# Kernel tuning notes

Hardware: AMD Instinct MI355X
Metric: run time of the kernel (lower is better)

Reference implementation:

```python
import jax, jax.numpy as jnp
import numpy as np

K = 2  # max_diffusion_step
UNITS = 128
NUM_NODES = 1024


def _diffusion_conv(x, support, W, b):
    # x: (B, N, D) ; Chebyshev diffusion over scaled Laplacian support (N, N)
    x0 = x
    x1 = jnp.einsum('nm,bmd->bnd', support, x0)
    xs = [x0, x1]
    for _ in range(K - 1):
        xs.append(2.0 * jnp.einsum('nm,bmd->bnd', support, xs[-1]) - xs[-2])
    feats = jnp.concatenate(xs, axis=-1)  # (B, N, D*(K+1))
    return feats @ W + b


def _gclstm_cell(x, h, c, support, W, b):
    gates = _diffusion_conv(jnp.concatenate([x, h], axis=-1), support, W, b)
    i, f, o, g = jnp.split(gates, 4, axis=-1)
    c_new = jax.nn.sigmoid(f) * c + jax.nn.sigmoid(i) * jnp.tanh(g)
    h_new = jax.nn.sigmoid(o) * jnp.tanh(c_new)
    return h_new, c_new


def setup_inputs() -> dict:
    key = jax.random.key(0)
    ks = jax.random.split(key, 8)
    B, S, N, H = 64, 12, NUM_NODES, UNITS

    # build scaled-Laplacian support from a sparse random symmetric adjacency
    rng = np.random.default_rng(0)
    A = (rng.random((N, N)) < 0.01).astype(np.float32)
    A = np.maximum(A, A.T)
    np.fill_diagonal(A, 0.0)
    d = A.sum(axis=1)
    d_is = 1.0 / np.sqrt(np.maximum(d, 1.0))
    L = np.eye(N, dtype=np.float32) - (d_is[:, None] * A * d_is[None, :])
    support = (L - np.eye(N, dtype=np.float32)).astype(np.float32)  # lambda_max ~ 2

    def lin(k, shape, fan_in):
        return jax.random.normal(k, shape, jnp.float32) / np.sqrt(fan_in)

    return {
        'inputs': jax.random.normal(ks[0], (B, N, 1), jnp.float32),
        'encoder_outputs': jax.random.normal(ks[1], (S, B, N, H), jnp.float32),
        'hidden_state': jax.random.normal(ks[2], (2, B, N, H), jnp.float32),
        'cell_state': jax.random.normal(ks[3], (2, B, N, H), jnp.float32),
        'supports': jnp.asarray(support),
        'w0': lin(ks[4], ((1 + H) * (K + 1), 4 * H), (1 + H) * (K + 1)),
        'b0': jnp.zeros((4 * H,), jnp.float32),
        'w1': lin(ks[5], ((H + H) * (K + 1), 4 * H), 2 * H * (K + 1)),
        'b1': jnp.zeros((4 * H,), jnp.float32),
        'attn_w': lin(ks[6], (H, H), H),
        'attn_b': jnp.zeros((H,), jnp.float32),
        'proj_w': lin(ks[7], (2 * H, 1), 2 * H),
        'proj_b': jnp.zeros((1,), jnp.float32),
    }


def reference(inputs, encoder_outputs, hidden_state, cell_state, supports,
              w0, b0, w1, b1, attn_w, attn_b, proj_w, proj_b):
    out = inputs
    hs, cs = [], []
    for layer, (W, b) in enumerate([(w0, b0), (w1, b1)]):
        h_new, c_new = _gclstm_cell(out, hidden_state[layer], cell_state[layer],
                                    supports, W, b)
        hs.append(h_new)
        cs.append(c_new)
        out = h_new  # (B, N, H)

    # additive attention: energy (S,B,N) -> softmax over S
    energy = jnp.tanh(encoder_outputs @ attn_w + attn_b)          # (S,B,N,H)
    energy = jnp.sum(energy * out[None], axis=-1)                 # (S,B,N)
    attention_weights = jax.nn.softmax(jnp.transpose(energy, (1, 2, 0)), axis=-1)  # (B,N,S)

    # bmm context gather
    context = jnp.einsum('bns,sbnh->bnh', attention_weights, encoder_outputs)

    cat = jnp.concatenate([out, context], axis=-1)                # (B,N,2H)
    projected = cat @ proj_w + proj_b                             # (B,N,out_dim)
    B = out.shape[0]
    output = projected.reshape(B, -1)                             # (B, N*out_dim)
    return output, jnp.stack(hs), jnp.stack(cs), attention_weights
```

## Files before the change

kernel.cpp:

```cpp
#include <hip/hip_runtime.h>
#include <hip/hip_bf16.h>
#include <stdint.h>

#define NB 64
#define NN 1024
#define NH 128
#define NS 12
#define BN (NB*NN)
#define D0 129
#define K0P 416
#define K1 768
#define NG 512
#define MAXNNZ 128
#define CH 16384
#define NCHUNK (BN/CH)

typedef __hip_bfloat16 bf16;
typedef float v4f __attribute__((ext_vector_type(4)));
typedef __bf16 v8bf __attribute__((ext_vector_type(8)));

__device__ __forceinline__ float bf2f(bf16 x) { return __bfloat162float(x); }
__device__ __forceinline__ bf16 f2bf(float x) { return __float2bfloat16(x); }
__device__ __forceinline__ float sane(float x) { return __builtin_isfinite(x) ? x : 0.f; }
__device__ __forceinline__ float sigf(float x) { return 1.f / (1.f + __expf(-x)); }
__device__ __forceinline__ float tanhfast(float x) { return 1.f - 2.f / (1.f + __expf(2.f * x)); }

__device__ __forceinline__ float loadF(const void* p, size_t i, int f32) {
  return f32 ? ((const float*)p)[i] : bf2f(((const bf16*)p)[i]);
}
__device__ __forceinline__ void storeF(void* p, size_t i, float v, int f32) {
  if (f32) ((float*)p)[i] = v; else ((bf16*)p)[i] = f2bf(v);
}
__device__ __forceinline__ v8bf load8(const void* p, size_t i, int f32) {
  if (f32) {
    const float4 a = *(const float4*)((const float*)p + i);
    const float4 b = *(const float4*)((const float*)p + i + 4);
    union { v8bf v; __hip_bfloat162 h[4]; } u;
    u.h[0] = __float22bfloat162_rn(make_float2(a.x, a.y));
    u.h[1] = __float22bfloat162_rn(make_float2(a.z, a.w));
    u.h[2] = __float22bfloat162_rn(make_float2(b.x, b.y));
    u.h[3] = __float22bfloat162_rn(make_float2(b.z, b.w));
    return u.v;
  }
  return *(const v8bf*)((const bf16*)p + i);
}

__global__ void detect_dtype(const unsigned short* __restrict__ probe, int* __restrict__ flag) {
  int t = threadIdx.x;
  unsigned short x = probe[2 * t];
  int e = (x >> 7) & 0xFF;
  int insane = !((x & 0x7FFF) == 0 || (e >= 117 && e <= 131));
  __shared__ int cnt;
  if (t == 0) cnt = 0;
  __syncthreads();
  atomicAdd(&cnt, insane);
  __syncthreads();
  if (t == 0) *flag = (cnt > 64) ? 1 : 0;
}

__global__ void build_csr(const void* __restrict__ sup, int* __restrict__ cols,
                          float* __restrict__ vals, int* __restrict__ cnt,
                          const int* __restrict__ flag) {
  int f32 = *flag;
  int n = blockIdx.x;
  __shared__ int cn;
  if (threadIdx.x == 0) cn = 0;
  __syncthreads();
  for (int m = threadIdx.x; m < NN; m += blockDim.x) {
    float v = loadF(sup, (size_t)n * NN + m, f32);
    if (v != 0.0f && __builtin_isfinite(v)) {
      int slot = atomicAdd(&cn, 1);
      if (slot < MAXNNZ) { cols[n * MAXNNZ + slot] = m; vals[n * MAXNNZ + slot] = v; }
    }
  }
  __syncthreads();
  if (threadIdx.x == 0) cnt[n] = (cn < MAXNNZ) ? cn : MAXNNZ;
}

__global__ void pack_wt(const void* __restrict__ w, bf16* __restrict__ bt,
                        int K, int Kp, int Nn, const int* __restrict__ flag) {
  int f32 = *flag;
  int n = blockIdx.x;
  for (int k = threadIdx.x; k < Kp; k += blockDim.x) {
    float v = (k < K) ? loadF(w, (size_t)k * Nn + n, f32) : 0.0f;
    bt[(size_t)n * Kp + k] = f2bf(v);
  }
}

__global__ void diffuse0_a(const void* __restrict__ xin, const void* __restrict__ h0,
                           const int* __restrict__ cols, const float* __restrict__ vals,
                           const int* __restrict__ cnt, bf16* __restrict__ feats,
                           const int* __restrict__ flag, int R) {
  int f32 = *flag;
  int bn = R + blockIdx.x;
  int lbn = blockIdx.x;
  int n = bn & (NN - 1);
  int b = bn >> 10;
  int d = threadIdx.x;
  bf16* frow = feats + (size_t)lbn * K0P;
  if (d < D0) {
    float x0 = (d == 0) ? loadF(xin, bn, f32) : loadF(h0, (size_t)bn * NH + d - 1, f32);
    frow[d] = f2bf(x0);
    float acc = 0.f;
    int c = cnt[n];
    for (int j = 0; j < c; ++j) {
      int m = cols[n * MAXNNZ + j];
      float s = vals[n * MAXNNZ + j];
      int bm = (b << 10) | m;
      float xv = (d == 0) ? loadF(xin, bm, f32) : loadF(h0, (size_t)bm * NH + d - 1, f32);
      acc += s * xv;
    }
    frow[D0 + d] = f2bf(acc);
  } else if (d < D0 + (K0P - 3 * D0)) {
    frow[3 * D0 + (d - D0)] = f2bf(0.f);
  }
}

__global__ void diffuse0_b(const void* __restrict__ xin, const void* __restrict__ h0,
                           const int* __restrict__ cols, const float* __restrict__ vals,
                           const int* __restrict__ cnt, bf16* __restrict__ feats,
                           const int* __restrict__ flag, int R) {
  int f32 = *flag;
  int bn = R + blockIdx.x;
  int lbn = blockIdx.x;
  int n = bn & (NN - 1);
  int b = bn >> 10;
  int d = threadIdx.x;
  if (d >= D0) return;
  float x0 = (d == 0) ? loadF(xin, bn, f32) : loadF(h0, (size_t)bn * NH + d - 1, f32);
  float acc = -x0;
  int c = cnt[n];
  for (int j = 0; j < c; ++j) {
    int m = cols[n * MAXNNZ + j];
    float s = vals[n * MAXNNZ + j];
    int lbm = ((b << 10) | m) - R;
    float x1 = bf2f(feats[(size_t)lbm * K0P + D0 + d]);
    acc += 2.f * s * x1;
  }
  feats[(size_t)lbn * K0P + 2 * D0 + d] = f2bf(acc);
}

__global__ void diffuse1_a(const void* __restrict__ dout, size_t offH0,
                           const void* __restrict__ hidden, size_t offH1in,
                           const int* __restrict__ cols, const float* __restrict__ vals,
                           const int* __restrict__ cnt, bf16* __restrict__ feats,
                           const int* __restrict__ flag, int R) {
  int f32 = *flag;
  int bn = R + blockIdx.x;
  int lbn = blockIdx.x;
  int n = bn & (NN - 1);
  int b = bn >> 10;
  int d = threadIdx.x;
  bf16* frow = feats + (size_t)lbn * K1;
  float x0 = (d < NH) ? loadF(dout, offH0 + (size_t)bn * NH + d, f32)
                      : loadF(hidden, offH1in + (size_t)bn * NH + d - NH, f32);
  frow[d] = f2bf(x0);
  float acc = 0.f;
  int c = cnt[n];
  for (int j = 0; j < c; ++j) {
    int m = cols[n * MAXNNZ + j];
    float s = vals[n * MAXNNZ + j];
    size_t bm = (size_t)((b << 10) | m) * NH;
    float xv = (d < NH) ? loadF(dout, offH0 + bm + d, f32)
                        : loadF(hidden, offH1in + bm + d - NH, f32);
    acc += s * xv;
  }
  frow[256 + d] = f2bf(acc);
}

__global__ void diffuse1_b(const void* __restrict__ dout, size_t offH0,
                           const void* __restrict__ hidden, size_t offH1in,
                           const int* __restrict__ cols, const float* __restrict__ vals,
                           const int* __restrict__ cnt, bf16* __restrict__ feats,
                           const int* __restrict__ flag, int R) {
  int f32 = *flag;
  int bn = R + blockIdx.x;
  int lbn = blockIdx.x;
  int n = bn & (NN - 1);
  int b = bn >> 10;
  int d = threadIdx.x;
  float x0 = (d < NH) ? loadF(dout, offH0 + (size_t)bn * NH + d, f32)
                      : loadF(hidden, offH1in + (size_t)bn * NH + d - NH, f32);
  float acc = -x0;
  int c = cnt[n];
  for (int j = 0; j < c; ++j) {
    int m = cols[n * MAXNNZ + j];
    float s = vals[n * MAXNNZ + j];
    int lbm = ((b << 10) | m) - R;
    float x1 = bf2f(feats[(size_t)lbm * K1 + 256 + d]);
    acc += 2.f * s * x1;
  }
  feats[(size_t)lbn * K1 + 512 + d] = f2bf(acc);
}

__global__ __launch_bounds__(256) void gemm_bt(const bf16* __restrict__ A,
    const bf16* __restrict__ Bt, const void* __restrict__ bias,
    bf16* __restrict__ C, int Kd, const int* __restrict__ flag) {
  int f32 = *flag;
  __shared__ __align__(16) unsigned short As[128 * 32];
  __shared__ __align__(16) unsigned short Bs[128 * 32];
  const int tid = threadIdx.x;
  const int l = tid & 63;
  const int w = tid >> 6;
  const int wm = w >> 1, wn = w & 1;
  const int m0 = blockIdx.x * 128;
  const int n0 = blockIdx.y * 128;
  const bf16* Ab = A + (size_t)m0 * Kd;
  const bf16* Bb = Bt + (size_t)n0 * Kd;
  const int lr = l & 15, q = l >> 4;
  v4f acc[4][4] = {};
  for (int k0 = 0; k0 < Kd; k0 += 32) {
    v8bf ga[2], gb[2];
#pragma unroll
    for (int t = 0; t < 2; ++t) {
      int s = tid + 256 * t;
      int row = s >> 2, col = (s & 3) * 8;
      ga[t] = *(const v8bf*)(Ab + (size_t)row * Kd + k0 + col);
      gb[t] = *(const v8bf*)(Bb + (size_t)row * Kd + k0 + col);
    }
    __syncthreads();
#pragma unroll
    for (int t = 0; t < 2; ++t) {
      int s = tid + 256 * t;
      int row = s >> 2, col = (s & 3) * 8;
      *(v8bf*)&As[row * 32 + col] = ga[t];
      *(v8bf*)&Bs[row * 32 + col] = gb[t];
    }
    __syncthreads();
    v8bf af[4], bfv[4];
#pragma unroll
    for (int i = 0; i < 4; ++i) {
      af[i]  = *(const v8bf*)&As[(wm * 64 + i * 16 + lr) * 32 + q * 8];
      bfv[i] = *(const v8bf*)&Bs[(wn * 64 + i * 16 + lr) * 32 + q * 8];
    }
#pragma unroll
    for (int mt = 0; mt < 4; ++mt)
#pragma unroll
      for (int nt = 0; nt < 4; ++nt)
        acc[mt][nt] = __builtin_amdgcn_mfma_f32_16x16x32_bf16(af[mt], bfv[nt], acc[mt][nt], 0, 0, 0);
    __syncthreads();
  }
#pragma unroll
  for (int nt = 0; nt < 4; ++nt) {
    int n = n0 + wn * 64 + nt * 16 + lr;
    float bv = loadF(bias, n, f32);
#pragma unroll
    for (int mt = 0; mt < 4; ++mt)
#pragma unroll
      for (int r = 0; r < 4; ++r) {
        int m = m0 + wm * 64 + mt * 16 + q * 4 + r;
        C[(size_t)m * NG + n] = f2bf(acc[mt][nt][r] + bv);
      }
  }
}

#define BPAD 136
__global__ __launch_bounds__(256) void gemm_energy(const void* __restrict__ enc,
    const bf16* __restrict__ Bt, const void* __restrict__ bias,
    const void* __restrict__ dout, size_t offH1, float* __restrict__ energy,
    const int* __restrict__ flag) {
  int f32 = *flag;
  __shared__ __align__(16) unsigned short As[128 * 32];
  __shared__ __align__(16) unsigned short Bsf[128 * BPAD];
  __shared__ float ered[2][128];
  const int tid = threadIdx.x;
  const int l = tid & 63;
  const int w = tid >> 6;
  const int wm = w >> 1, wn = w & 1;
  const int m0 = blockIdx.x * 128;
  const int lr = l & 15, q = l >> 4;

#pragma unroll
  for (int i = tid; i < 2048; i += 256) {
    int row = i >> 4, chunk = i & 15;
    *(v8bf*)&Bsf[row * BPAD + chunk * 8] = *(const v8bf*)(Bt + (size_t)row * NH + chunk * 8);
  }

  v4f acc[4][4] = {};
  for (int k0 = 0; k0 < NH; k0 += 32) {
    v8bf ga[2];
#pragma unroll
    for (int t = 0; t < 2; ++t) {
      int s = tid + 256 * t;
      int row = s >> 2, col = (s & 3) * 8;
      ga[t] = load8(enc, (size_t)(m0 + row) * NH + k0 + col, f32);
    }
    __syncthreads();
#pragma unroll
    for (int t = 0; t < 2; ++t) {
      int s = tid + 256 * t;
      int row = s >> 2, col = (s & 3) * 8;
      *(v8bf*)&As[row * 32 + col] = ga[t];
    }
    __syncthreads();
    v8bf af[4], bfv[4];
#pragma unroll
    for (int i = 0; i < 4; ++i) {
      af[i]  = *(const v8bf*)&As[(wm * 64 + i * 16 + lr) * 32 + q * 8];
      bfv[i] = *(const v8bf*)&Bsf[(wn * 64 + i * 16 + lr) * BPAD + k0 + q * 8];
    }
#pragma unroll
    for (int mt = 0; mt < 4; ++mt)
#pragma unroll
      for (int nt = 0; nt < 4; ++nt)
        acc[mt][nt] = __builtin_amdgcn_mfma_f32_16x16x32_bf16(af[mt], bfv[nt], acc[mt][nt], 0, 0, 0);
    __syncthreads();
  }
#pragma unroll
  for (int mt = 0; mt < 4; ++mt) {
    float parts[4] = {0.f, 0.f, 0.f, 0.f};
#pragma unroll
    for (int nt = 0; nt < 4; ++nt) {
      int n = wn * 64 + nt * 16 + lr;
      float bv = loadF(bias, n, f32);
#pragma unroll
      for (int r = 0; r < 4; ++r) {
        int m = m0 + wm * 64 + mt * 16 + q * 4 + r;
        int bn = m & (BN - 1);
        float t = tanhfast(acc[mt][nt][r] + bv);
        parts[r] += t * loadF(dout, offH1 + (size_t)bn * NH + n, f32);
      }
    }
#pragma unroll
    for (int r = 0; r < 4; ++r) {
      float v = parts[r];
      v += __shfl_xor(v, 1);
      v += __shfl_xor(v, 2);
      v += __shfl_xor(v, 4);
      v += __shfl_xor(v, 8);
      if (lr == 0) {
        int lm = wm * 64 + mt * 16 + q * 4 + r;
        ered[wn][lm] = v;
      }
    }
  }
  __syncthreads();
  if (tid < 128) energy[m0 + tid] = sane(ered[0][tid] + ered[1][tid]);
}

__global__ __launch_bounds__(128) void lstm_cell(const bf16* __restrict__ gates,
    const void* __restrict__ cell, size_t offCin, void* __restrict__ dout,
    size_t offH, size_t offC, const int* __restrict__ flag, int R) {
  int f32 = *flag;
  size_t lbn = blockIdx.x;
  size_t bn = (size_t)R + lbn;
  int h = threadIdx.x;
  const bf16* g = gates + lbn * NG;
  float iv = sane(bf2f(g[h]));
  float fv = sane(bf2f(g[NH + h]));
  float ov = sane(bf2f(g[2 * NH + h]));
  float gv = sane(bf2f(g[3 * NH + h]));
  float c = sane(loadF(cell, offCin + bn * NH + h, f32));
  float cn = sigf(fv) * c + sigf(iv) * tanhfast(gv);
  float hn = sigf(ov) * tanhfast(cn);
  storeF(dout, offC + bn * NH + h, cn, f32);
  storeF(dout, offH + bn * NH + h, hn, f32);
}

__global__ void softmax_s(const float* __restrict__ energy, float* __restrict__ attnf,
                          void* __restrict__ dout, size_t offAttn,
                          const int* __restrict__ flag) {
  int f32 = *flag;
  int bn = blockIdx.x * blockDim.x + threadIdx.x;
  float e[NS];
  float mx = -3.4e38f;
#pragma unroll
  for (int s = 0; s < NS; ++s) { e[s] = sane(energy[s * BN + bn]); mx = fmaxf(mx, e[s]); }
  float sum = 0.f;
#pragma unroll
  for (int s = 0; s < NS; ++s) { e[s] = __expf(e[s] - mx); sum += e[s]; }
  float inv = 1.f / sum;
#pragma unroll
  for (int s = 0; s < NS; ++s) {
    float wv = e[s] * inv;
    attnf[(size_t)bn * NS + s] = wv;
    storeF(dout, offAttn + (size_t)bn * NS + s, wv, f32);
  }
}

__global__ __launch_bounds__(256) void context_proj(const void* __restrict__ enc,
    const float* __restrict__ attnf, void* __restrict__ dout, size_t offH1,
    const void* __restrict__ proj_w, const void* __restrict__ proj_b,
    const int* __restrict__ flag) {
  int f32 = *flag;
  int sub = threadIdx.x >> 7;
  int h = threadIdx.x & 127;
  int bn = blockIdx.x * 2 + sub;
  float ctx = 0.f;
#pragma unroll
  for (int s = 0; s < NS; ++s) {
    float aw = attnf[(size_t)bn * NS + s];
    ctx += aw * loadF(enc, ((size_t)s * BN + bn) * NH + h, f32);
  }
  float ov = loadF(dout, offH1 + (size_t)bn * NH + h, f32);
  float part = sane(ov * loadF(proj_w, h, f32) + ctx * loadF(proj_w, NH + h, f32));
#pragma unroll
  for (int mask = 1; mask < 64; mask <<= 1) part += __shfl_xor(part, mask);
  __shared__ float red[4];
  if ((threadIdx.x & 63) == 0) red[threadIdx.x >> 6] = part;
  __syncthreads();
  if (h == 0) storeF(dout, bn, red[sub * 2] + red[sub * 2 + 1] + loadF(proj_b, 0, f32), f32);
}

extern "C" void kernel_launch(void* const* d_in, const int* in_sizes, int n_in,
                              void* d_out, int out_size, void* d_ws, size_t ws_size,
                              hipStream_t stream) {
  const void* xin    = d_in[0];
  const void* enc    = d_in[1];
  const void* hidden = d_in[2];
  const void* cell   = d_in[3];
  const void* sup    = d_in[4];
  const void* w0     = d_in[5];
  const void* b0     = d_in[6];
  const void* w1     = d_in[7];
  const void* b1     = d_in[8];
  const void* aw     = d_in[9];
  const void* ab     = d_in[10];
  const void* pw     = d_in[11];
  const void* pb     = d_in[12];

  char* ws = (char*)d_ws;
  size_t off = 0;
  auto alloc = [&](size_t bytes) -> char* {
    char* p = ws + off;
    off += (bytes + 255) & ~(size_t)255;
    return p;
  };
  bf16*  feats    = (bf16*)alloc((size_t)CH * K1 * 2);
  bf16*  gates    = (bf16*)alloc((size_t)CH * NG * 2);
  float* energy   = (float*)alloc((size_t)NS * BN * 4);
  float* attnf    = (float*)alloc((size_t)BN * NS * 4);
  bf16*  Bt0      = (bf16*)alloc((size_t)NG * K0P * 2);
  bf16*  Bt1      = (bf16*)alloc((size_t)NG * K1 * 2);
  bf16*  BtA      = (bf16*)alloc((size_t)NH * NH * 2);
  int*   csr_cols = (int*)alloc((size_t)NN * MAXNNZ * 4);
  float* csr_vals = (float*)alloc((size_t)NN * MAXNNZ * 4);
  int*   csr_cnt  = (int*)alloc((size_t)NN * 4);
  int*   flag     = (int*)alloc(256);

  const size_t OFF_HS   = (size_t)BN;
  const size_t OFF_CS   = OFF_HS + (size_t)2 * BN * NH;
  const size_t OFF_ATTN = OFF_CS + (size_t)2 * BN * NH;
  const size_t OFF_H0 = OFF_HS;
  const size_t OFF_H1 = OFF_HS + (size_t)BN * NH;
  const size_t OFF_C0 = OFF_CS;
  const size_t OFF_C1 = OFF_CS + (size_t)BN * NH;
  const size_t LAYER1 = (size_t)BN * NH;

  detect_dtype<<<1, 256, 0, stream>>>((const unsigned short*)cell, flag);
  build_csr<<<NN, 256, 0, stream>>>(sup, csr_cols, csr_vals, csr_cnt, flag);
  pack_wt<<<NG, 256, 0, stream>>>(w0, Bt0, 387, K0P, NG, flag);
  pack_wt<<<NG, 256, 0, stream>>>(w1, Bt1, K1, K1, NG, flag);
  pack_wt<<<NH, 128, 0, stream>>>(aw, BtA, NH, NH, NH, flag);

  for (int c = 0; c < NCHUNK; ++c) {
    int R = c * CH;
    diffuse0_a<<<CH, 192, 0, stream>>>(xin, hidden, csr_cols, csr_vals, csr_cnt, feats, flag, R);
    diffuse0_b<<<CH, 192, 0, stream>>>(xin, hidden, csr_cols, csr_vals, csr_cnt, feats, flag, R);
    dim3 g(CH / 128, NG / 128);
    gemm_bt<<<g, 256, 0, stream>>>(feats, Bt0, b0, gates, K0P, flag);
    lstm_cell<<<CH, 128, 0, stream>>>(gates, cell, 0, d_out, OFF_H0, OFF_C0, flag, R);
  }

  for (int c = 0; c < NCHUNK; ++c) {
    int R = c * CH;
    diffuse1_a<<<CH, 256, 0, stream>>>(d_out, OFF_H0, hidden, LAYER1,
                                       csr_cols, csr_vals, csr_cnt, feats, flag, R);
    diffuse1_b<<<CH, 256, 0, stream>>>(d_out, OFF_H0, hidden, LAYER1,
                                       csr_cols, csr_vals, csr_cnt, feats, flag, R);
    dim3 g(CH / 128, NG / 128);
    gemm_bt<<<g, 256, 0, stream>>>(feats, Bt1, b1, gates, K1, flag);
    lstm_cell<<<CH, 128, 0, stream>>>(gates, cell, LAYER1, d_out, OFF_H1, OFF_C1, flag, R);
  }

  gemm_energy<<<NS * BN / 128, 256, 0, stream>>>(enc, BtA, ab, d_out, OFF_H1, energy, flag);
  softmax_s<<<BN / 256, 256, 0, stream>>>(energy, attnf, d_out, OFF_ATTN, flag);
  context_proj<<<BN / 2, 256, 0, stream>>>(enc, attnf, d_out, OFF_H1, pw, pb, flag);
}
```

Before: 1.969 ms.

## Fuse attention energy, softmax and context into one kernel; drop chunking

Replaces the three-kernel attention tail (energy GEMM, softmax, context/projection) with a single kernel. Each block stages 8 node-rows of encoder outputs for all 12 steps in shared memory and computes energy via MFMA, softmax, context and projection on chip, so the encoder tensor is read once instead of twice and the energy/attention intermediates never go to global memory. It also removes the 4-chunk loop over batch-node rows so each diffusion, GEMM and LSTM kernel launches once over the full problem. The cost is larger feats/gates workspace buffers. The attention kernel also uses small MFMA tiles that leave half the rows unused.

```diff
diff --git a/kernel.cpp b/kernel.cpp
--- a/kernel.cpp
+++ b/kernel.cpp
@@ -12,8 +12,6 @@
 #define K1 768
 #define NG 512
 #define MAXNNZ 128
-#define CH 16384
-#define NCHUNK (BN/CH)
 
 typedef __hip_bfloat16 bf16;
 typedef float v4f __attribute__((ext_vector_type(4)));
@@ -90,14 +88,13 @@
 __global__ void diffuse0_a(const void* __restrict__ xin, const void* __restrict__ h0,
                            const int* __restrict__ cols, const float* __restrict__ vals,
                            const int* __restrict__ cnt, bf16* __restrict__ feats,
-                           const int* __restrict__ flag, int R) {
-  int f32 = *flag;
-  int bn = R + blockIdx.x;
-  int lbn = blockIdx.x;
+                           const int* __restrict__ flag) {
+  int f32 = *flag;
+  int bn = blockIdx.x;
   int n = bn & (NN - 1);
   int b = bn >> 10;
   int d = threadIdx.x;
-  bf16* frow = feats + (size_t)lbn * K0P;
+  bf16* frow = feats + (size_t)bn * K0P;
   if (d < D0) {
     float x0 = (d == 0) ? loadF(xin, bn, f32) : loadF(h0, (size_t)bn * NH + d - 1, f32);
     frow[d] = f2bf(x0);
@@ -119,10 +116,9 @@
 __global__ void diffuse0_b(const void* __restrict__ xin, const void* __restrict__ h0,
                            const int* __restrict__ cols, const float* __restrict__ vals,
                            const int* __restrict__ cnt, bf16* __restrict__ feats,
-                           const int* __restrict__ flag, int R) {
-  int f32 = *flag;
-  int bn = R + blockIdx.x;
-  int lbn = blockIdx.x;
+                           const int* __restrict__ flag) {
+  int f32 = *flag;
+  int bn = blockIdx.x;
   int n = bn & (NN - 1);
   int b = bn >> 10;
   int d = threadIdx.x;
@@ -133,25 +129,24 @@
   for (int j = 0; j < c; ++j) {
     int m = cols[n * MAXNNZ + j];
     float s = vals[n * MAXNNZ + j];
-    int lbm = ((b << 10) | m) - R;
-    float x1 = bf2f(feats[(size_t)lbm * K0P + D0 + d]);
+    int bm = (b << 10) | m;
+    float x1 = bf2f(feats[(size_t)bm * K0P + D0 + d]);
     acc += 2.f * s * x1;
   }
-  feats[(size_t)lbn * K0P + 2 * D0 + d] = f2bf(acc);
+  feats[(size_t)bn * K0P + 2 * D0 + d] = f2bf(acc);
 }
 
 __global__ void diffuse1_a(const void* __restrict__ dout, size_t offH0,
                            const void* __restrict__ hidden, size_t offH1in,
                            const int* __restrict__ cols, const float* __restrict__ vals,
                            const int* __restrict__ cnt, bf16* __restrict__ feats,
-                           const int* __restrict__ flag, int R) {
-  int f32 = *flag;
-  int bn = R + blockIdx.x;
-  int lbn = blockIdx.x;
+                           const int* __restrict__ flag) {
+  int f32 = *flag;
+  int bn = blockIdx.x;
   int n = bn & (NN - 1);
   int b = bn >> 10;
   int d = threadIdx.x;
-  bf16* frow = feats + (size_t)lbn * K1;
+  bf16* frow = feats + (size_t)bn * K1;
   float x0 = (d < NH) ? loadF(dout, offH0 + (size_t)bn * NH + d, f32)
                       : loadF(hidden, offH1in + (size_t)bn * NH + d - NH, f32);
   frow[d] = f2bf(x0);
@@ -172,10 +167,9 @@
                            const void* __restrict__ hidden, size_t offH1in,
                            const int* __restrict__ cols, const float* __restrict__ vals,
                            const int* __restrict__ cnt, bf16* __restrict__ feats,
-                           const int* __restrict__ flag, int R) {
-  int f32 = *flag;
-  int bn = R + blockIdx.x;
-  int lbn = blockIdx.x;
+                           const int* __restrict__ flag) {
+  int f32 = *flag;
+  int bn = blockIdx.x;
   int n = bn & (NN - 1);
   int b = bn >> 10;
   int d = threadIdx.x;
@@ -186,11 +180,11 @@
   for (int j = 0; j < c; ++j) {
     int m = cols[n * MAXNNZ + j];
     float s = vals[n * MAXNNZ + j];
-    int lbm = ((b << 10) | m) - R;
-    float x1 = bf2f(feats[(size_t)lbm * K1 + 256 + d]);
+    int bm = (b << 10) | m;
+    float x1 = bf2f(feats[(size_t)bm * K1 + 256 + d]);
     acc += 2.f * s * x1;
   }
-  feats[(size_t)lbn * K1 + 512 + d] = f2bf(acc);
+  feats[(size_t)bn * K1 + 512 + d] = f2bf(acc);
 }
 
 __global__ __launch_bounds__(256) void gemm_bt(const bf16* __restrict__ A,
@@ -254,98 +248,13 @@
   }
 }
 
-#define BPAD 136
-__global__ __launch_bounds__(256) void gemm_energy(const void* __restrict__ enc,
-    const bf16* __restrict__ Bt, const void* __restrict__ bias,
-    const void* __restrict__ dout, size_t offH1, float* __restrict__ energy,
-    const int* __restrict__ flag) {
-  int f32 = *flag;
-  __shared__ __align__(16) unsigned short As[128 * 32];
-  __shared__ __align__(16) unsigned short Bsf[128 * BPAD];
-  __shared__ float ered[2][128];
-  const int tid = threadIdx.x;
-  const int l = tid & 63;
-  const int w = tid >> 6;
-  const int wm = w >> 1, wn = w & 1;
-  const int m0 = blockIdx.x * 128;
-  const int lr = l & 15, q = l >> 4;
-
-#pragma unroll
-  for (int i = tid; i < 2048; i += 256) {
-    int row = i >> 4, chunk = i & 15;
-    *(v8bf*)&Bsf[row * BPAD + chunk * 8] = *(const v8bf*)(Bt + (size_t)row * NH + chunk * 8);
-  }
-
-  v4f acc[4][4] = {};
-  for (int k0 = 0; k0 < NH; k0 += 32) {
-    v8bf ga[2];
-#pragma unroll
-    for (int t = 0; t < 2; ++t) {
-      int s = tid + 256 * t;
-      int row = s >> 2, col = (s & 3) * 8;
-      ga[t] = load8(enc, (size_t)(m0 + row) * NH + k0 + col, f32);
-    }
-    __syncthreads();
-#pragma unroll
-    for (int t = 0; t < 2; ++t) {
-      int s = tid + 256 * t;
-      int row = s >> 2, col = (s & 3) * 8;
-      *(v8bf*)&As[row * 32 + col] = ga[t];
-    }
-    __syncthreads();
-    v8bf af[4], bfv[4];
-#pragma unroll
-    for (int i = 0; i < 4; ++i) {
-      af[i]  = *(const v8bf*)&As[(wm * 64 + i * 16 + lr) * 32 + q * 8];
-      bfv[i] = *(const v8bf*)&Bsf[(wn * 64 + i * 16 + lr) * BPAD + k0 + q * 8];
-    }
-#pragma unroll
-    for (int mt = 0; mt < 4; ++mt)
-#pragma unroll
-      for (int nt = 0; nt < 4; ++nt)
-        acc[mt][nt] = __builtin_amdgcn_mfma_f32_16x16x32_bf16(af[mt], bfv[nt], acc[mt][nt], 0, 0, 0);
-    __syncthreads();
-  }
-#pragma unroll
-  for (int mt = 0; mt < 4; ++mt) {
-    float parts[4] = {0.f, 0.f, 0.f, 0.f};
-#pragma unroll
-    for (int nt = 0; nt < 4; ++nt) {
-      int n = wn * 64 + nt * 16 + lr;
-      float bv = loadF(bias, n, f32);
-#pragma unroll
-      for (int r = 0; r < 4; ++r) {
-        int m = m0 + wm * 64 + mt * 16 + q * 4 + r;
-        int bn = m & (BN - 1);
-        float t = tanhfast(acc[mt][nt][r] + bv);
-        parts[r] += t * loadF(dout, offH1 + (size_t)bn * NH + n, f32);
-      }
-    }
-#pragma unroll
-    for (int r = 0; r < 4; ++r) {
-      float v = parts[r];
-      v += __shfl_xor(v, 1);
-      v += __shfl_xor(v, 2);
-      v += __shfl_xor(v, 4);
-      v += __shfl_xor(v, 8);
-      if (lr == 0) {
-        int lm = wm * 64 + mt * 16 + q * 4 + r;
-        ered[wn][lm] = v;
-      }
-    }
-  }
-  __syncthreads();
-  if (tid < 128) energy[m0 + tid] = sane(ered[0][tid] + ered[1][tid]);
-}
-
 __global__ __launch_bounds__(128) void lstm_cell(const bf16* __restrict__ gates,
     const void* __restrict__ cell, size_t offCin, void* __restrict__ dout,
-    size_t offH, size_t offC, const int* __restrict__ flag, int R) {
-  int f32 = *flag;
-  size_t lbn = blockIdx.x;
-  size_t bn = (size_t)R + lbn;
+    size_t offH, size_t offC, const int* __restrict__ flag) {
+  int f32 = *flag;
+  size_t bn = blockIdx.x;
   int h = threadIdx.x;
-  const bf16* g = gates + lbn * NG;
+  const bf16* g = gates + bn * NG;
   float iv = sane(bf2f(g[h]));
   float fv = sane(bf2f(g[NH + h]));
   float ov = sane(bf2f(g[2 * NH + h]));
@@ -357,49 +266,119 @@
   storeF(dout, offH + bn * NH + h, hn, f32);
 }
 
-__global__ void softmax_s(const float* __restrict__ energy, float* __restrict__ attnf,
-                          void* __restrict__ dout, size_t offAttn,
-                          const int* __restrict__ flag) {
-  int f32 = *flag;
-  int bn = blockIdx.x * blockDim.x + threadIdx.x;
-  float e[NS];
-  float mx = -3.4e38f;
-#pragma unroll
-  for (int s = 0; s < NS; ++s) { e[s] = sane(energy[s * BN + bn]); mx = fmaxf(mx, e[s]); }
-  float sum = 0.f;
-#pragma unroll
-  for (int s = 0; s < NS; ++s) { e[s] = __expf(e[s] - mx); sum += e[s]; }
-  float inv = 1.f / sum;
-#pragma unroll
+#define AROWS 8
+#define EPADF 132
+__global__ __launch_bounds__(512) void fused_attn(const void* __restrict__ enc,
+    const bf16* __restrict__ BtW, const void* __restrict__ ab,
+    void* __restrict__ dout, size_t offH1, size_t offAttn,
+    const void* __restrict__ pw, const void* __restrict__ pb,
+    const int* __restrict__ flag) {
+  int f32 = *flag;
+  __shared__ __align__(16) float encsf[(NS * AROWS + 8) * EPADF];
+  __shared__ float h1s[AROWS][NH];
+  __shared__ float ered[NS][8][AROWS];
+  __shared__ float wts[NS][AROWS];
+  const int tid = threadIdx.x;
+  const int l = tid & 63, w = tid >> 6;
+  const int bn0 = blockIdx.x * AROWS;
+
+  for (int i = tid; i < 8 * EPADF; i += 512) encsf[NS * AROWS * EPADF + i] = 0.f;
+  for (int g = tid; g < NS * AROWS * (NH / 4); g += 512) {
+    int s = g >> 8;
+    int r = (g >> 5) & 7;
+    int cg = g & 31;
+    float4 v;
+    if (f32) {
+      v = *(const float4*)((const float*)enc + ((size_t)s * BN + bn0 + r) * NH + cg * 4);
+    } else {
+      const bf16* p = (const bf16*)enc + ((size_t)s * BN + bn0 + r) * NH + cg * 4;
+      v = make_float4(bf2f(p[0]), bf2f(p[1]), bf2f(p[2]), bf2f(p[3]));
+    }
+    *(float4*)&encsf[(s * AROWS + r) * EPADF + cg * 4] = v;
+  }
+  for (int i = tid; i < AROWS * NH; i += 512) {
+    int r = i >> 7, h = i & 127;
+    h1s[r][h] = loadF(dout, offH1 + (size_t)(bn0 + r) * NH + h, f32);
+  }
+  __syncthreads();
+
+  const int lr = l & 15, q = l >> 4;
+  const int n = w * 16 + lr;
+  const float bvs = loadF(ab, n, f32);
   for (int s = 0; s < NS; ++s) {
-    float wv = e[s] * inv;
-    attnf[(size_t)bn * NS + s] = wv;
-    storeF(dout, offAttn + (size_t)bn * NS + s, wv, f32);
-  }
-}
-
-__global__ __launch_bounds__(256) void context_proj(const void* __restrict__ enc,
-    const float* __restrict__ attnf, void* __restrict__ dout, size_t offH1,
-    const void* __restrict__ proj_w, const void* __restrict__ proj_b,
-    const int* __restrict__ flag) {
-  int f32 = *flag;
-  int sub = threadIdx.x >> 7;
-  int h = threadIdx.x & 127;
-  int bn = blockIdx.x * 2 + sub;
-  float ctx = 0.f;
-#pragma unroll
-  for (int s = 0; s < NS; ++s) {
-    float aw = attnf[(size_t)bn * NS + s];
-    ctx += aw * loadF(enc, ((size_t)s * BN + bn) * NH + h, f32);
-  }
-  float ov = loadF(dout, offH1 + (size_t)bn * NH + h, f32);
-  float part = sane(ov * loadF(proj_w, h, f32) + ctx * loadF(proj_w, NH + h, f32));
-#pragma unroll
-  for (int mask = 1; mask < 64; mask <<= 1) part += __shfl_xor(part, mask);
-  __shared__ float red[4];
-  if ((threadIdx.x & 63) == 0) red[threadIdx.x >> 6] = part;
-  __syncthreads();
-  if (h == 0) storeF(dout, bn, red[sub * 2] + red[sub * 2 + 1] + loadF(proj_b, 0, f32), f32);
+    v4f acc = {};
+#pragma unroll
+    for (int kk = 0; kk < 4; ++kk) {
+      const float* ap = &encsf[(s * AROWS + lr) * EPADF + kk * 32 + q * 8];
+      float4 a0 = *(const float4*)ap;
+      float4 a1 = *(const float4*)(ap + 4);
+      union { v8bf v; __hip_bfloat162 h[4]; } ua;
+      ua.h[0] = __float22bfloat162_rn(make_float2(a0.x, a0.y));
+      ua.h[1] = __float22bfloat162_rn(make_float2(a0.z, a0.w));
+      ua.h[2] = __float22bfloat162_rn(make_float2(a1.x, a1.y));
+      ua.h[3] = __float22bfloat162_rn(make_float2(a1.z, a1.w));
+      v8bf bv = *(const v8bf*)(BtW + (size_t)n * NH + kk * 32 + q * 8);
+      acc = __builtin_amdgcn_mfma_f32_16x16x32_bf16(ua.v, bv, acc, 0, 0, 0);
+    }
+    float parts[4];
+#pragma unroll
+    for (int r = 0; r < 4; ++r) {
+      int m = q * 4 + r;
+      float t = tanhfast(acc[r] + bvs);
+      parts[r] = (m < AROWS) ? t * h1s[m][n] : 0.f;
+    }
+#pragma unroll
+    for (int r = 0; r < 4; ++r) {
+      float v = parts[r];
+      v += __shfl_xor(v, 1);
+      v += __shfl_xor(v, 2);
+      v += __shfl_xor(v, 4);
+      v += __shfl_xor(v, 8);
+      int m = q * 4 + r;
+      if (lr == 0 && m < AROWS) ered[s][w][m] = v;
+    }
+  }
+  __syncthreads();
+  if (tid < AROWS) {
+    int m = tid;
+    float e[NS];
+    float mx = -3.4e38f;
+#pragma unroll
+    for (int s = 0; s < NS; ++s) {
+      float v = 0.f;
+#pragma unroll
+      for (int ww = 0; ww < 8; ++ww) v += ered[s][ww][m];
+      e[s] = sane(v);
+      mx = fmaxf(mx, e[s]);
+    }
+    float sum = 0.f;
+#pragma unroll
+    for (int s = 0; s < NS; ++s) { e[s] = __expf(e[s] - mx); sum += e[s]; }
+    float inv = 1.f / sum;
+#pragma unroll
+    for (int s = 0; s < NS; ++s) wts[s][m] = e[s] * inv;
+  }
+  __syncthreads();
+  if (tid < AROWS * NS) {
+    int m = tid / NS, s = tid - m * NS;
+    storeF(dout, offAttn + (size_t)(bn0 + m) * NS + s, wts[s][m], f32);
+  }
+  {
+    int m = w;
+    float part = 0.f;
+#pragma unroll
+    for (int hh = 0; hh < 2; ++hh) {
+      int h = l + hh * 64;
+      float ctx = 0.f;
+#pragma unroll
+      for (int s = 0; s < NS; ++s)
+        ctx += wts[s][m] * encsf[(s * AROWS + m) * EPADF + h];
+      part += sane(h1s[m][h] * loadF(pw, h, f32) + ctx * loadF(pw, NH + h, f32));
+    }
+#pragma unroll
+    for (int mask = 1; mask < 64; mask <<= 1) part += __shfl_xor(part, mask);
+    if (l == 0) storeF(dout, bn0 + m, part + loadF(pb, 0, f32), f32);
+  }
 }
 
 extern "C" void kernel_launch(void* const* d_in, const int* in_sizes, int n_in,
@@ -426,10 +405,8 @@
     off += (bytes + 255) & ~(size_t)255;
     return p;
   };
-  bf16*  feats    = (bf16*)alloc((size_t)CH * K1 * 2);
-  bf16*  gates    = (bf16*)alloc((size_t)CH * NG * 2);
-  float* energy   = (float*)alloc((size_t)NS * BN * 4);
-  float* attnf    = (float*)alloc((size_t)BN * NS * 4);
+  bf16*  feats    = (bf16*)alloc((size_t)BN * K1 * 2);
+  bf16*  gates    = (bf16*)alloc((size_t)BN * NG * 2);
   bf16*  Bt0      = (bf16*)alloc((size_t)NG * K0P * 2);
   bf16*  Bt1      = (bf16*)alloc((size_t)NG * K1 * 2);
   bf16*  BtA      = (bf16*)alloc((size_t)NH * NH * 2);
@@ -453,27 +430,24 @@
   pack_wt<<<NG, 256, 0, stream>>>(w1, Bt1, K1, K1, NG, flag);
   pack_wt<<<NH, 128, 0, stream>>>(aw, BtA, NH, NH, NH, flag);
 
-  for (int c = 0; c < NCHUNK; ++c) {
-    int R = c * CH;
-    diffuse0_a<<<CH, 192, 0, stream>>>(xin, hidden, csr_cols, csr_vals, csr_cnt, feats, flag, R);
-    diffuse0_b<<<CH, 192, 0, stream>>>(xin, hidden, csr_cols, csr_vals, csr_cnt, feats, flag, R);
-    dim3 g(CH / 128, NG / 128);
+  diffuse0_a<<<BN, 192, 0, stream>>>(xin, hidden, csr_cols, csr_vals, csr_cnt, feats, flag);
+  diffuse0_b<<<BN, 192, 0, stream>>>(xin, hidden, csr_cols, csr_vals, csr_cnt, feats, flag);
+  {
+    dim3 g(BN / 128, NG / 128);
     gemm_bt<<<g, 256, 0, stream>>>(feats, Bt0, b0, gates, K0P, flag);
-    lstm_cell<<<CH, 128, 0, stream>>>(gates, cell, 0, d_out, OFF_H0, OFF_C0, flag, R);
-  }
-
-  for (int c = 0; c < NCHUNK; ++c) {
-    int R = c * CH;
-    diffuse1_a<<<CH, 256, 0, stream>>>(d_out, OFF_H0, hidden, LAYER1,
-                                       csr_cols, csr_vals, csr_cnt, feats, flag, R);
-    diffuse1_b<<<CH, 256, 0, stream>>>(d_out, OFF_H0, hidden, LAYER1,
-                                       csr_cols, csr_vals, csr_cnt, feats, flag, R);
-    dim3 g(CH / 128, NG / 128);
+  }
+  lstm_cell<<<BN, 128, 0, stream>>>(gates, cell, 0, d_out, OFF_H0, OFF_C0, flag);
+
+  diffuse1_a<<<BN, 256, 0, stream>>>(d_out, OFF_H0, hidden, LAYER1,
+                                     csr_cols, csr_vals, csr_cnt, feats, flag);
+  diffuse1_b<<<BN, 256, 0, stream>>>(d_out, OFF_H0, hidden, LAYER1,
+                                     csr_cols, csr_vals, csr_cnt, feats, flag);
+  {
+    dim3 g(BN / 128, NG / 128);
     gemm_bt<<<g, 256, 0, stream>>>(feats, Bt1, b1, gates, K1, flag);
-    lstm_cell<<<CH, 128, 0, stream>>>(gates, cell, LAYER1, d_out, OFF_H1, OFF_C1, flag, R);
-  }
-
-  gemm_energy<<<NS * BN / 128, 256, 0, stream>>>(enc, BtA, ab, d_out, OFF_H1, energy, flag);
-  softmax_s<<<BN / 256, 256, 0, stream>>>(energy, attnf, d_out, OFF_ATTN, flag);
-  context_proj<<<BN / 2, 256, 0, stream>>>(enc, attnf, d_out, OFF_H1, pw, pb, flag);
-}
+  }
+  lstm_cell<<<BN, 128, 0, stream>>>(gates, cell, LAYER1, d_out, OFF_H1, OFF_C1, flag);
+
+  fused_attn<<<BN / AROWS, 512, 0, stream>>>(enc, BtA, ab, d_out, OFF_H1, OFF_ATTN,
+                                             pw, pb, flag);
+}
```

Result: slower. 2.110 ms (+7.2%).
